# Optimization experiments

Measured on AMD Instinct MI355X. Metric: run time of the kernel, lower is better.

The kernel has to match this reference:

```python
import jax, jax.numpy as jnp
import numpy as np

B, T, NF, D, H = 4, 32, 256, 512, 8
DK = D // H


def setup_inputs() -> dict:
    key = jax.random.key(0)
    ks = jax.random.split(key, 10)
    x = jax.random.normal(ks[0], (B, T, NF, D), dtype=jnp.float32)
    adj = jax.random.randint(ks[1], (NF, NF), 0, 2, dtype=jnp.int32)
    adj = adj.at[jnp.arange(NF), jnp.arange(NF)].set(1)  # self-loops avoid all-masked rows
    s = 1.0 / np.sqrt(D)
    Wq = jax.random.normal(ks[2], (D, D), dtype=jnp.float32) * s
    Wk = jax.random.normal(ks[3], (D, D), dtype=jnp.float32) * s
    Wv = jax.random.normal(ks[4], (D, D), dtype=jnp.float32) * s
    Wo = jax.random.normal(ks[5], (D, D), dtype=jnp.float32) * s
    bq = jnp.zeros((D,), jnp.float32)
    bk = jnp.zeros((D,), jnp.float32)
    bv = jnp.zeros((D,), jnp.float32)
    bo = jnp.zeros((D,), jnp.float32)
    return {"x": x, "adj": adj, "Wq": Wq, "bq": bq, "Wk": Wk, "bk": bk,
            "Wv": Wv, "bv": bv, "Wo": Wo, "bo": bo}


def reference(x, adj, Wq, bq, Wk, bk, Wv, bv, Wo, bo):
    b, t, nf, d = x.shape
    q = x @ Wq.T + bq
    k = x @ Wk.T + bk
    v = x @ Wv.T + bv
    # split heads: [B,T,Nf,H,dk]
    qh = q.reshape(b, t, nf, H, DK)
    kh = k.reshape(b, t, nf, H, DK)
    vh = v.reshape(b, t, nf, H, DK)
    scores = jnp.einsum('btihd,btjhd->bthij', qh, kh) / jnp.sqrt(jnp.float32(DK))
    mask = (adj > 0)  # [Nf,Nf], broadcast over b,t,h
    scores = jnp.where(mask[None, None, None], scores, jnp.float32(-jnp.inf))
    attn = jax.nn.softmax(scores, axis=-1)  # dropout is identity in eval
    out = jnp.einsum('bthij,btjhd->btihd', attn, vh).reshape(b, t, nf, d)
    return out @ Wo.T + bo
```

## Files before the change

kernel.cpp:

```cpp
#include <hip/hip_runtime.h>

#define NF 256
#define H_ 8
#define M_ 32768

typedef _Float16 f16;
typedef _Float16 f16x8 __attribute__((ext_vector_type(8)));
typedef float f32x4 __attribute__((ext_vector_type(4)));
typedef unsigned short u16x8 __attribute__((ext_vector_type(8)));

#define GLOAD16(src, dst) \
  __builtin_amdgcn_global_load_lds((const __attribute__((address_space(1))) void*)(src), \
                                   (__attribute__((address_space(3))) void*)(dst), 16, 0, 0)

#define LDS_FENCE() do { asm volatile("s_waitcnt lgkmcnt(0)" ::: "memory"); \
                         __builtin_amdgcn_sched_barrier(0); } while (0)
#define SBAR() asm volatile("s_barrier" ::: "memory")


__device__ __forceinline__ void stageHT(const f16* __restrict__ g, int r0, int k0,
                                        f16* ldst, int wave, int lane) {
    const int key = lane >> 3;
    const int colsw = k0 + (((lane & 7) ^ key) << 3);
#pragma unroll
    for (int i = 0; i < 2; ++i) {
        int r = i * 64 + wave * 8 + key;
        GLOAD16(g + (size_t)(r0 + r) * 512 + colsw, ldst + (i * 64 + wave * 8) * 64);
    }
}

__device__ __forceinline__ void gemm256_core(const f16* __restrict__ A, const f16* __restrict__ W,
                                             int m0, int n0, f16* lds,
                                             f32x4 (&acc)[8][4], int wave, int lane) {
    const int wr = wave & 1, wc = wave >> 1;
    const int l15 = lane & 15, l4 = lane >> 4;
    stageHT(W, n0,        0, lds + 16384, wave, lane);
    stageHT(W, n0 + 128,  0, lds + 24576, wave, lane);
    stageHT(A, m0,        0, lds,         wave, lane);
    stageHT(A, m0 + 128,  0, lds + 8192,  wave, lane);
    stageHT(W, n0,       64, lds + 32768 + 16384, wave, lane);
    stageHT(W, n0 + 128, 64, lds + 32768 + 24576, wave, lane);
    asm volatile("s_waitcnt vmcnt(4)" ::: "memory");
    SBAR();
#pragma unroll
    for (int t = 0; t < 8; ++t) {
        f16* bufA = lds + (t & 1) * 32768;
        f16* bufB = bufA + 16384;
        f16* nA   = lds + ((t & 1) ^ 1) * 32768;
        f16x8 bfr[4][2];
#pragma unroll
        for (int j = 0; j < 4; ++j)
#pragma unroll
            for (int kk = 0; kk < 2; ++kk) {
                int rb = wc * 64 + j * 16 + l15;
                bfr[j][kk] = *reinterpret_cast<const f16x8*>(
                    bufB + rb * 64 + ((((kk << 2) + l4) ^ (rb & 7)) << 3));
            }
#pragma unroll
        for (int q = 0; q < 4; ++q) {
            f16x8 afr[2][2];
#pragma unroll
            for (int rf = 0; rf < 2; ++rf)
#pragma unroll
                for (int kk = 0; kk < 2; ++kk) {
                    int ra = wr * 128 + q * 32 + rf * 16 + l15;
                    afr[rf][kk] = *reinterpret_cast<const f16x8*>(
                        bufA + ra * 64 + ((((kk << 2) + l4) ^ (ra & 7)) << 3));
                }
            if (q == 0 && t < 7) stageHT(A, m0,       (t + 1) * 64, nA,          wave, lane);
            if (q == 1 && t < 7) stageHT(A, m0 + 128, (t + 1) * 64, nA + 8192,   wave, lane);
            if (q == 2 && t < 6) stageHT(W, n0,       (t + 2) * 64, bufB,        wave, lane);
            if (q == 3 && t < 6) stageHT(W, n0 + 128, (t + 2) * 64, bufB + 8192, wave, lane);
            SBAR();
            LDS_FENCE();
            __builtin_amdgcn_s_setprio(1);
#pragma unroll
            for (int rf = 0; rf < 2; ++rf)
#pragma unroll
                for (int j = 0; j < 4; ++j)
#pragma unroll
                    for (int kk = 0; kk < 2; ++kk)
                        acc[q * 2 + rf][j] = __builtin_amdgcn_mfma_f32_16x16x32_f16(
                            afr[rf][kk], bfr[j][kk], acc[q * 2 + rf][j], 0, 0, 0);
            __builtin_amdgcn_s_setprio(0);
            if (q < 3) SBAR();
        }
        if (t < 6) { asm volatile("s_waitcnt vmcnt(4)" ::: "memory"); }
        else       { asm volatile("s_waitcnt vmcnt(0)" ::: "memory"); }
        SBAR();
    }
}


#define QSCALE 0.1803368801111204f

__global__ void prep_all(const float* __restrict__ x, f16* __restrict__ xh,
                         const float* __restrict__ Wq, const float* __restrict__ Wk,
                         const float* __restrict__ Wv, const float* __restrict__ Wo,
                         const float* __restrict__ bq, const float* __restrict__ bk,
                         const float* __restrict__ bv, const int* __restrict__ adj,
                         f16* __restrict__ Wh, f16* __restrict__ Woh,
                         float* __restrict__ biasAll, unsigned long long* __restrict__ bmask) {
    if (blockIdx.x < 2048) {
        int idx = blockIdx.x * 256 + threadIdx.x;
        for (; idx < M_ * 512 / 8; idx += 2048 * 256) {
            const float4* s = reinterpret_cast<const float4*>(x + (size_t)idx * 8);
            float4 v0 = s[0], v1 = s[1];
            f16x8 o;
            o[0] = (f16)v0.x; o[1] = (f16)v0.y; o[2] = (f16)v0.z; o[3] = (f16)v0.w;
            o[4] = (f16)v1.x; o[5] = (f16)v1.y; o[6] = (f16)v1.z; o[7] = (f16)v1.w;
            *reinterpret_cast<f16x8*>(xh + (size_t)idx * 8) = o;
        }
        return;
    }
    const int tid = (blockIdx.x - 2048) * 256 + threadIdx.x;
    {
        const float* s; f16* d; float sc = 1.0f;
        int pp = tid >> 15, off = tid & 32767;
        if (pp == 0)      { s = Wq; d = Wh;              sc = QSCALE; }
        else if (pp == 1) { s = Wk; d = Wh + 512 * 512; }
        else if (pp == 2) { s = Wv; d = Wh + 2 * 512 * 512; }
        else              { s = Wo; d = Woh; }
        const float4* sv4 = reinterpret_cast<const float4*>(s + (size_t)off * 8);
        float4 v0 = sv4[0], v1 = sv4[1];
        f16x8 o;
        o[0] = (f16)(v0.x * sc); o[1] = (f16)(v0.y * sc);
        o[2] = (f16)(v0.z * sc); o[3] = (f16)(v0.w * sc);
        o[4] = (f16)(v1.x * sc); o[5] = (f16)(v1.y * sc);
        o[6] = (f16)(v1.z * sc); o[7] = (f16)(v1.w * sc);
        *reinterpret_cast<f16x8*>(d + (size_t)off * 8) = o;
    }
    if (tid < 1536) {
        float v = (tid < 512) ? QSCALE * bq[tid] : (tid < 1024) ? bk[tid - 512] : bv[tid - 1024];
        biasAll[tid] = v;
    }
    if (tid < 65536) {
        unsigned long long bal = __ballot(adj[tid] > 0);
        if ((tid & 63) == 0) bmask[tid >> 6] = bal;
    }
}


__global__ __launch_bounds__(512) void qkv_gemm(const f16* __restrict__ A, const f16* __restrict__ W,
                                                const float* __restrict__ biasAll,
                                                f16* __restrict__ out) {
    __shared__ __align__(16) f16 lds[65536];
    const int tt = threadIdx.x, wave = tt >> 6, lane = tt & 63;
    const int lb = blockIdx.x, xcd = lb & 7, idx = lb >> 3;
    const int m0 = (xcd * 16 + idx / 6) * 256;
    const int n0 = (idx % 6) * 256;
    f32x4 acc[8][4] = {};
    gemm256_core(A, W, m0, n0, lds, acc, wave, lane);

    const int wr = wave & 1, wc = wave >> 1;
    const int l15 = lane & 15, l4 = lane >> 4;
    f16* epi = lds;
    float bb[4];
#pragma unroll
    for (int bc = 0; bc < 4; ++bc) bb[bc] = biasAll[n0 + wc * 64 + bc * 16 + l15];
#pragma unroll
    for (int half = 0; half < 2; ++half) {
        if (wr == half) {
#pragma unroll
            for (int ar = 0; ar < 8; ++ar)
#pragma unroll
                for (int bc = 0; bc < 4; ++bc)
#pragma unroll
                    for (int r = 0; r < 4; ++r)
                        epi[(ar * 16 + l4 * 4 + r) * 264 + wc * 64 + bc * 16 + l15] =
                            (f16)(acc[ar][bc][r] + bb[bc]);
        }
        LDS_FENCE();
        SBAR();
        const int rr = tt >> 5, slot = tt & 31;
#pragma unroll
        for (int p = 0; p < 8; ++p) {
            int row = p * 16 + rr;
            *reinterpret_cast<f16x8*>(out + (size_t)(m0 + half * 128 + row) * 1536 + n0 + slot * 8) =
                *reinterpret_cast<const f16x8*>(epi + row * 264 + slot * 8);
        }
        SBAR();
    }
}


template <int NR>
__device__ __forceinline__ void stage_rows512(const f16* __restrict__ g, int ld, int coff,
                                              f16* ldsb, int wave, int lane) {
    const int rr = wave * 8 + (lane >> 3);
    const int p  = lane & 7;
#pragma unroll
    for (int i = 0; i < NR / 64; ++i) {
        int r = i * 64 + rr;
        int col = ((p ^ (r & 7)) << 3);
        GLOAD16(g + (size_t)r * ld + coff + col, ldsb + (i * 64 + wave * 8) * 64);
    }
}

__global__ __launch_bounds__(512) void attn_kernel(const f16* __restrict__ qkv,
                                                   const unsigned long long* __restrict__ bmg,
                                                   f16* __restrict__ ao) {
    __shared__ f16 Ks[256 * 64];
    __shared__ f16 Vs[64 * 256];
    __shared__ f16 Ps[8][16][264];
    __shared__ unsigned long long BMs[1024];
    const int t = threadIdx.x, wave = t >> 6, lane = t & 63;
    const int l15 = lane & 15, l4 = lane >> 4;
    const int bh = blockIdx.x, bt = bh >> 3, h = bh & 7;
    const int btq = bt * 256, hq = h * 64;
    const f16* qb = qkv + (size_t)btq * 1536 + hq;
    const f16* kb = qkv + (size_t)btq * 1536 + 512 + hq;
    const f16* vb = qkv + (size_t)btq * 1536 + 1024 + hq;

    stage_rows512<256>(kb, 1536, 0, Ks, wave, lane);
    GLOAD16((const char*)bmg + (size_t)t * 16, (char*)(BMs + wave * 128));
    {
        const int slot = t & 7, r0 = t >> 3;
#pragma unroll
        for (int i = 0; i < 4; ++i) {
            int nf = r0 + i * 64;
            f16x8 v = *reinterpret_cast<const f16x8*>(vb + (size_t)nf * 1536 + slot * 8);
#pragma unroll
            for (int e = 0; e < 8; ++e) {
                int dk = slot * 8 + e;
                int key = (dk & 7) ^ (dk >> 3);
                Vs[dk * 256 + (((nf >> 3) ^ key) << 3) + (nf & 7)] = v[e];
            }
        }
    }
    __syncthreads();

    for (int s = 0; s < 2; ++s) {
        const int qrow_base = wave * 32 + s * 16;

        f16x8 aq[2];
#pragma unroll
        for (int kk = 0; kk < 2; ++kk)
            aq[kk] = *reinterpret_cast<const f16x8*>(
                qb + (size_t)(qrow_base + l15) * 1536 + kk * 32 + l4 * 8);

        f32x4 sacc[16];
#pragma unroll
        for (int ct = 0; ct < 16; ++ct) sacc[ct] = (f32x4){0.f, 0.f, 0.f, 0.f};
#pragma unroll
        for (int ct = 0; ct < 16; ++ct)
#pragma unroll
            for (int kk = 0; kk < 2; ++kk) {
                int rk = ct * 16 + l15;
                int sk = kk * 4 + l4;
                f16x8 bk_ = *reinterpret_cast<const f16x8*>(Ks + rk * 64 + ((sk ^ (rk & 7)) << 3));
                sacc[ct] = __builtin_amdgcn_mfma_f32_16x16x32_f16(aq[kk], bk_, sacc[ct], 0, 0, 0);
            }

        LDS_FENCE();

        float rs[4];
#pragma unroll
        for (int r = 0; r < 4; ++r) {
            const int ig = qrow_base + l4 * 4 + r;
            const u16x8* mr = reinterpret_cast<const u16x8*>(BMs + ig * 4);
            u16x8 w0 = mr[0], w1 = mr[1];
            float mx = -1e38f;
#pragma unroll
            for (int ct = 0; ct < 16; ++ct) mx = fmaxf(mx, sacc[ct][r]);
#pragma unroll
            for (int m = 1; m < 16; m <<= 1) mx = fmaxf(mx, __shfl_xor(mx, m, 64));
            float sum = 0.f;
#pragma unroll
            for (int ct = 0; ct < 16; ++ct) {
                unsigned wbit = (ct < 8) ? (unsigned)w0[ct] : (unsigned)w1[ct & 7];
                float p = __builtin_exp2f(sacc[ct][r] - mx);
                p = ((wbit >> l15) & 1u) ? p : 0.0f;
                sacc[ct][r] = p;
                sum += p;
            }
#pragma unroll
            for (int m = 1; m < 16; m <<= 1) sum += __shfl_xor(sum, m, 64);
            rs[r] = 1.0f / sum;
#pragma unroll
            for (int ct = 0; ct < 16; ++ct)
                Ps[wave][l4 * 4 + r][ct * 16 + l15] = (f16)sacc[ct][r];
        }

        LDS_FENCE();

        f32x4 oacc[4] = {};
#pragma unroll
        for (int kk = 0; kk < 8; ++kk) {
            f16x8 ap = *reinterpret_cast<const f16x8*>(&Ps[wave][l15][kk * 32 + l4 * 8]);
#pragma unroll
            for (int c2 = 0; c2 < 4; ++c2) {
                int dk = c2 * 16 + l15;
                int key = (dk & 7) ^ (dk >> 3);
                int sv = kk * 4 + l4;
                f16x8 bv_ = *reinterpret_cast<const f16x8*>(Vs + dk * 256 + ((sv ^ key) << 3));
                oacc[c2] = __builtin_amdgcn_mfma_f32_16x16x32_f16(ap, bv_, oacc[c2], 0, 0, 0);
            }
        }
#pragma unroll
        for (int c2 = 0; c2 < 4; ++c2)
#pragma unroll
            for (int r = 0; r < 4; ++r) {
                int nf = qrow_base + l4 * 4 + r;
                int dcol = hq + c2 * 16 + l15;
                ao[((size_t)btq + nf) * 512 + dcol] = (f16)(oacc[c2][r] * rs[r]);
            }
    }
}


__global__ __launch_bounds__(512) void o_gemm(const f16* __restrict__ A, const f16* __restrict__ W,
                                              const float* __restrict__ bo, float* __restrict__ out) {
    __shared__ __align__(16) f16 lds[65536];
    const int tt = threadIdx.x, wave = tt >> 6, lane = tt & 63;
    const int lb = blockIdx.x, xcd = lb & 7, idx = lb >> 3;
    const int m0 = (xcd * 16 + idx / 2) * 256;
    const int n0 = (idx % 2) * 256;
    f32x4 acc[8][4] = {};
    gemm256_core(A, W, m0, n0, lds, acc, wave, lane);

    const int wr = wave & 1, wc = wave >> 1;
    const int l15 = lane & 15, l4 = lane >> 4;
    float bb[4];
#pragma unroll
    for (int bc = 0; bc < 4; ++bc) bb[bc] = bo[n0 + wc * 64 + bc * 16 + l15];
#pragma unroll
    for (int ar = 0; ar < 8; ++ar)
#pragma unroll
        for (int bc = 0; bc < 4; ++bc) {
            int ng = n0 + wc * 64 + bc * 16 + l15;
#pragma unroll
            for (int r = 0; r < 4; ++r) {
                int mg = m0 + wr * 128 + ar * 16 + l4 * 4 + r;
                out[(size_t)mg * 512 + ng] = acc[ar][bc][r] + bb[bc];
            }
        }
}


extern "C" void kernel_launch(void* const* d_in, const int* in_sizes, int n_in,
                              void* d_out, int out_size, void* d_ws, size_t ws_size,
                              hipStream_t stream) {
    const float* x   = (const float*)d_in[0];
    const int*   adj = (const int*)d_in[1];
    const float* Wq  = (const float*)d_in[2];
    const float* bq  = (const float*)d_in[3];
    const float* Wk  = (const float*)d_in[4];
    const float* bk  = (const float*)d_in[5];
    const float* Wv  = (const float*)d_in[6];
    const float* bv  = (const float*)d_in[7];
    const float* Wo  = (const float*)d_in[8];
    const float* bo  = (const float*)d_in[9];
    float* out = (float*)d_out;

    char* ws = (char*)d_ws;
    f16*   Wh      = (f16*)ws;
    f16*   Woh     = (f16*)(ws + 1572864);
    float* biasAll = (float*)(ws + 2097152);
    unsigned long long* bmask = (unsigned long long*)(ws + 2103296);
    f16*   xh      = (f16*)(ws + 2111488);
    f16*   qkvb    = (f16*)(ws + 2111488 + (size_t)M_ * 512 * 2);
    f16*   aob     = xh;

    prep_all<<<2560, 256, 0, stream>>>(x, xh, Wq, Wk, Wv, Wo, bq, bk, bv, adj,
                                       Wh, Woh, biasAll, bmask);
    qkv_gemm<<<768, 512, 0, stream>>>(xh, Wh, biasAll, qkvb);
    attn_kernel<<<128 * H_, 512, 0, stream>>>(qkvb, bmask, aob);
    o_gemm<<<256, 512, 0, stream>>>(aob, Woh, bo, out);
}
```

Measured before the change: 182.3 us.

## Write V transposed from QKV GEMM and keep attention probabilities in registers

The QKV GEMM epilogue now writes the V part pre-transposed per (b,t,head) into a separate buffer, so the attention kernel loads V with async global-to-LDS copies instead of scalar scattered LDS stores. Scores are computed as K·Q^T so each lane owns one query row, which removes most cross-lane reductions and lets the probabilities feed the PV MFMA straight from registers via packed fp16 conversion. This drops the Ps LDS buffer and allows an occupancy hint of 4 blocks. The costs are an uncoalesced, strided transpose in the GEMM epilogue and extra workspace.

```diff
diff --git a/kernel.cpp b/kernel.cpp
--- a/kernel.cpp
+++ b/kernel.cpp
@@ -5,6 +5,8 @@
 #define M_ 32768
 
 typedef _Float16 f16;
+typedef __fp16 fp16v2 __attribute__((ext_vector_type(2)));
+typedef _Float16 f16x4 __attribute__((ext_vector_type(4)));
 typedef _Float16 f16x8 __attribute__((ext_vector_type(8)));
 typedef float f32x4 __attribute__((ext_vector_type(4)));
 typedef unsigned short u16x8 __attribute__((ext_vector_type(8)));
@@ -143,7 +145,7 @@
 
 __global__ __launch_bounds__(512) void qkv_gemm(const f16* __restrict__ A, const f16* __restrict__ W,
                                                 const float* __restrict__ biasAll,
-                                                f16* __restrict__ out) {
+                                                f16* __restrict__ out, f16* __restrict__ vT) {
     __shared__ __align__(16) f16 lds[65536];
     const int tt = threadIdx.x, wave = tt >> 6, lane = tt & 63;
     const int lb = blockIdx.x, xcd = lb & 7, idx = lb >> 3;
@@ -155,6 +157,7 @@
     const int wr = wave & 1, wc = wave >> 1;
     const int l15 = lane & 15, l4 = lane >> 4;
     f16* epi = lds;
+    const bool isV = (n0 >= 1024);
     float bb[4];
 #pragma unroll
     for (int bc = 0; bc < 4; ++bc) bb[bc] = biasAll[n0 + wc * 64 + bc * 16 + l15];
@@ -172,12 +175,26 @@
         }
         LDS_FENCE();
         SBAR();
-        const int rr = tt >> 5, slot = tt & 31;
-#pragma unroll
-        for (int p = 0; p < 8; ++p) {
-            int row = p * 16 + rr;
-            *reinterpret_cast<f16x8*>(out + (size_t)(m0 + half * 128 + row) * 1536 + n0 + slot * 8) =
-                *reinterpret_cast<const f16x8*>(epi + row * 264 + slot * 8);
+        if (!isV) {
+            const int rr = tt >> 5, slot = tt & 31;
+#pragma unroll
+            for (int p = 0; p < 8; ++p) {
+                int row = p * 16 + rr;
+                *reinterpret_cast<f16x8*>(out + (size_t)(m0 + half * 128 + row) * 1024 + n0 + slot * 8) =
+                    *reinterpret_cast<const f16x8*>(epi + row * 264 + slot * 8);
+            }
+        } else {
+            f16* vdst = vT + (size_t)(m0 >> 8) * 8 * 64 * 256 + (size_t)(n0 - 1024) * 256;
+            const int col = tt & 255, rh = tt >> 8;
+#pragma unroll
+            for (int i = 0; i < 8; ++i) {
+                int c8 = rh * 8 + i;
+                f16x8 v;
+#pragma unroll
+                for (int e = 0; e < 8; ++e) v[e] = epi[(c8 * 8 + e) * 264 + col];
+                int nf0 = half * 128 + c8 * 8;
+                *reinterpret_cast<f16x8*>(vdst + (size_t)col * 256 + nf0) = v;
+            }
         }
         SBAR();
     }
@@ -197,37 +214,35 @@
     }
 }
 
-__global__ __launch_bounds__(512) void attn_kernel(const f16* __restrict__ qkv,
-                                                   const unsigned long long* __restrict__ bmg,
-                                                   f16* __restrict__ ao) {
+__device__ __forceinline__ void stage_v512(const f16* __restrict__ g, f16* ldsb,
+                                           int wave, int lane) {
+    const int rr = wave * 8 + (lane >> 3);
+    const int p  = lane & 7;
+#pragma unroll
+    for (int i = 0; i < 4; ++i) {
+        int r = i * 64 + rr;
+        int key = (r ^ (r >> 3)) & 7;
+        GLOAD16(g + (size_t)r * 64 + ((p ^ key) << 3), ldsb + (i * 64 + wave * 8) * 64);
+    }
+}
+
+__global__ __launch_bounds__(512, 4) void attn_kernel(const f16* __restrict__ qkv,
+                                                      const f16* __restrict__ vT,
+                                                      const unsigned long long* __restrict__ bmg,
+                                                      f16* __restrict__ ao) {
     __shared__ f16 Ks[256 * 64];
-    __shared__ f16 Vs[64 * 256];
-    __shared__ f16 Ps[8][16][264];
+    __shared__ f16 Vs[256 * 64];
     __shared__ unsigned long long BMs[1024];
     const int t = threadIdx.x, wave = t >> 6, lane = t & 63;
     const int l15 = lane & 15, l4 = lane >> 4;
     const int bh = blockIdx.x, bt = bh >> 3, h = bh & 7;
     const int btq = bt * 256, hq = h * 64;
-    const f16* qb = qkv + (size_t)btq * 1536 + hq;
-    const f16* kb = qkv + (size_t)btq * 1536 + 512 + hq;
-    const f16* vb = qkv + (size_t)btq * 1536 + 1024 + hq;
-
-    stage_rows512<256>(kb, 1536, 0, Ks, wave, lane);
+    const f16* qb = qkv + (size_t)btq * 1024 + hq;
+    const f16* kb = qb + 512;
+
+    stage_rows512<256>(kb, 1024, 0, Ks, wave, lane);
+    stage_v512(vT + (size_t)bh * 16384, Vs, wave, lane);
     GLOAD16((const char*)bmg + (size_t)t * 16, (char*)(BMs + wave * 128));
-    {
-        const int slot = t & 7, r0 = t >> 3;
-#pragma unroll
-        for (int i = 0; i < 4; ++i) {
-            int nf = r0 + i * 64;
-            f16x8 v = *reinterpret_cast<const f16x8*>(vb + (size_t)nf * 1536 + slot * 8);
-#pragma unroll
-            for (int e = 0; e < 8; ++e) {
-                int dk = slot * 8 + e;
-                int key = (dk & 7) ^ (dk >> 3);
-                Vs[dk * 256 + (((nf >> 3) ^ key) << 3) + (nf & 7)] = v[e];
-            }
-        }
-    }
     __syncthreads();
 
     for (int s = 0; s < 2; ++s) {
@@ -237,11 +252,11 @@
 #pragma unroll
         for (int kk = 0; kk < 2; ++kk)
             aq[kk] = *reinterpret_cast<const f16x8*>(
-                qb + (size_t)(qrow_base + l15) * 1536 + kk * 32 + l4 * 8);
-
-        f32x4 sacc[16];
-#pragma unroll
-        for (int ct = 0; ct < 16; ++ct) sacc[ct] = (f32x4){0.f, 0.f, 0.f, 0.f};
+                qb + (size_t)(qrow_base + l15) * 1024 + kk * 32 + l4 * 8);
+
+        f32x4 sc[16];
+#pragma unroll
+        for (int ct = 0; ct < 16; ++ct) sc[ct] = (f32x4){0.f, 0.f, 0.f, 0.f};
 #pragma unroll
         for (int ct = 0; ct < 16; ++ct)
 #pragma unroll
@@ -249,52 +264,62 @@
                 int rk = ct * 16 + l15;
                 int sk = kk * 4 + l4;
                 f16x8 bk_ = *reinterpret_cast<const f16x8*>(Ks + rk * 64 + ((sk ^ (rk & 7)) << 3));
-                sacc[ct] = __builtin_amdgcn_mfma_f32_16x16x32_f16(aq[kk], bk_, sacc[ct], 0, 0, 0);
-            }
-
-        LDS_FENCE();
-
-        float rs[4];
-#pragma unroll
-        for (int r = 0; r < 4; ++r) {
-            const int ig = qrow_base + l4 * 4 + r;
-            const u16x8* mr = reinterpret_cast<const u16x8*>(BMs + ig * 4);
-            u16x8 w0 = mr[0], w1 = mr[1];
-            float mx = -1e38f;
-#pragma unroll
-            for (int ct = 0; ct < 16; ++ct) mx = fmaxf(mx, sacc[ct][r]);
-#pragma unroll
-            for (int m = 1; m < 16; m <<= 1) mx = fmaxf(mx, __shfl_xor(mx, m, 64));
-            float sum = 0.f;
-#pragma unroll
-            for (int ct = 0; ct < 16; ++ct) {
-                unsigned wbit = (ct < 8) ? (unsigned)w0[ct] : (unsigned)w1[ct & 7];
-                float p = __builtin_exp2f(sacc[ct][r] - mx);
-                p = ((wbit >> l15) & 1u) ? p : 0.0f;
-                sacc[ct][r] = p;
+                sc[ct] = __builtin_amdgcn_mfma_f32_16x16x32_f16(bk_, aq[kk], sc[ct], 0, 0, 0);
+            }
+
+        const int ig = qrow_base + l15;
+        const u16x8* mr = reinterpret_cast<const u16x8*>(BMs + ig * 4);
+        u16x8 w0 = mr[0], w1 = mr[1];
+        float mx = -1e38f;
+#pragma unroll
+        for (int ct = 0; ct < 16; ++ct)
+#pragma unroll
+            for (int r = 0; r < 4; ++r) mx = fmaxf(mx, sc[ct][r]);
+        mx = fmaxf(mx, __shfl_xor(mx, 16, 64));
+        mx = fmaxf(mx, __shfl_xor(mx, 32, 64));
+        float sum = 0.f;
+#pragma unroll
+        for (int ct = 0; ct < 16; ++ct) {
+            unsigned mb = ((ct < 8) ? (unsigned)w0[ct] : (unsigned)w1[ct & 7]) >> (l4 * 4);
+#pragma unroll
+            for (int r = 0; r < 4; ++r) {
+                float p = __builtin_exp2f(sc[ct][r] - mx);
+                p = ((mb >> r) & 1u) ? p : 0.0f;
+                sc[ct][r] = p;
                 sum += p;
             }
-#pragma unroll
-            for (int m = 1; m < 16; m <<= 1) sum += __shfl_xor(sum, m, 64);
-            rs[r] = 1.0f / sum;
-#pragma unroll
-            for (int ct = 0; ct < 16; ++ct)
-                Ps[wave][l4 * 4 + r][ct * 16 + l15] = (f16)sacc[ct][r];
-        }
-
-        LDS_FENCE();
+        }
+        sum += __shfl_xor(sum, 16, 64);
+        sum += __shfl_xor(sum, 32, 64);
+        float rs = 1.0f / sum;
+
+        union { fp16v2 h2[32]; f16x8 h8[8]; } pu;
+#pragma unroll
+        for (int ct = 0; ct < 16; ++ct) {
+            pu.h2[2 * ct]     = __builtin_amdgcn_cvt_pkrtz(sc[ct][0], sc[ct][1]);
+            pu.h2[2 * ct + 1] = __builtin_amdgcn_cvt_pkrtz(sc[ct][2], sc[ct][3]);
+        }
+        float rsrow[4];
+#pragma unroll
+        for (int r = 0; r < 4; ++r) rsrow[r] = __shfl(rs, l4 * 4 + r, 64);
 
         f32x4 oacc[4] = {};
 #pragma unroll
-        for (int kk = 0; kk < 8; ++kk) {
-            f16x8 ap = *reinterpret_cast<const f16x8*>(&Ps[wave][l15][kk * 32 + l4 * 8]);
+        for (int kkp = 0; kkp < 8; ++kkp) {
+            f16x8 pa = pu.h8[kkp];
 #pragma unroll
             for (int c2 = 0; c2 < 4; ++c2) {
-                int dk = c2 * 16 + l15;
-                int key = (dk & 7) ^ (dk >> 3);
-                int sv = kk * 4 + l4;
-                f16x8 bv_ = *reinterpret_cast<const f16x8*>(Vs + dk * 256 + ((sv ^ key) << 3));
-                oacc[c2] = __builtin_amdgcn_mfma_f32_16x16x32_f16(ap, bv_, oacc[c2], 0, 0, 0);
+                int d = c2 * 16 + l15;
+                int nf0a = kkp * 32 + l4 * 4;
+                int nf0b = nf0a + 16;
+                int rvA = d * 4 + (nf0a >> 6), rvB = d * 4 + (nf0b >> 6);
+                int keyA = (rvA ^ (rvA >> 3)) & 7, keyB = (rvB ^ (rvB >> 3)) & 7;
+                union { f16x4 h4[2]; f16x8 h8; } bu;
+                bu.h4[0] = *reinterpret_cast<const f16x4*>(
+                    Vs + rvA * 64 + ((((nf0a >> 3) & 7) ^ keyA) << 3) + (nf0a & 7));
+                bu.h4[1] = *reinterpret_cast<const f16x4*>(
+                    Vs + rvB * 64 + ((((nf0b >> 3) & 7) ^ keyB) << 3) + (nf0b & 7));
+                oacc[c2] = __builtin_amdgcn_mfma_f32_16x16x32_f16(pa, bu.h8, oacc[c2], 0, 0, 0);
             }
         }
 #pragma unroll
@@ -303,7 +328,7 @@
             for (int r = 0; r < 4; ++r) {
                 int nf = qrow_base + l4 * 4 + r;
                 int dcol = hq + c2 * 16 + l15;
-                ao[((size_t)btq + nf) * 512 + dcol] = (f16)(oacc[c2][r] * rs[r]);
+                ao[((size_t)btq + nf) * 512 + dcol] = (f16)(oacc[c2][r] * rsrow[r]);
             }
     }
 }
@@ -360,11 +385,12 @@
     unsigned long long* bmask = (unsigned long long*)(ws + 2103296);
     f16*   xh      = (f16*)(ws + 2111488);
     f16*   qkvb    = (f16*)(ws + 2111488 + (size_t)M_ * 512 * 2);
+    f16*   vTb     = (f16*)(ws + 2111488 + (size_t)M_ * 512 * 2 + (size_t)M_ * 1024 * 2);
     f16*   aob     = xh;
 
     prep_all<<<2560, 256, 0, stream>>>(x, xh, Wq, Wk, Wv, Wo, bq, bk, bv, adj,
                                        Wh, Woh, biasAll, bmask);
-    qkv_gemm<<<768, 512, 0, stream>>>(xh, Wh, biasAll, qkvb);
-    attn_kernel<<<128 * H_, 512, 0, stream>>>(qkvb, bmask, aob);
+    qkv_gemm<<<768, 512, 0, stream>>>(xh, Wh, biasAll, qkvb, vTb);
+    attn_kernel<<<128 * H_, 512, 0, stream>>>(qkvb, vTb, bmask, aob);
     o_gemm<<<256, 512, 0, stream>>>(aob, Woh, bo, out);
 }
```

Result: slower. 450.3 us (+147.0%).
